# Optimization experiments

Hardware: AMD Instinct MI355X
Metric: run time of the kernel (lower is better)

Reference implementation:

```python
import jax, jax.numpy as jnp
import numpy as np

B, T, D, H, K, ED = 4, 1024, 512, 8, 30, 128
HD = D // H
SCALE = HD ** -0.5


def _ln(x, g, b, eps=1e-5):
    m = jnp.mean(x, axis=-1, keepdims=True)
    v = jnp.var(x, axis=-1, keepdims=True)
    return (x - m) / jnp.sqrt(v + eps) * g + b


def setup_inputs() -> dict:
    key = jax.random.key(0)
    ks = jax.random.split(key, 16)
    s = 0.02
    return {
        "h_V": jax.random.normal(ks[0], (B, T, D), jnp.float32),
        "k": jax.random.normal(ks[1], (B, T, D), jnp.float32),
        "v": jax.random.normal(ks[2], (B, T, D), jnp.float32),
        "E": jax.random.normal(ks[3], (B, T, K, ED), jnp.float32),
        "bias": jax.random.normal(ks[4], (B, T, T), jnp.float32),
        "Wq": jax.random.normal(ks[5], (D, D), jnp.float32) * s,
        "bq": jnp.zeros((D,), jnp.float32),
        "Wk": jax.random.normal(ks[6], (D, D), jnp.float32) * s,
        "bk": jnp.zeros((D,), jnp.float32),
        "Wv": jax.random.normal(ks[7], (D, D), jnp.float32) * s,
        "bv": jnp.zeros((D,), jnp.float32),
        "Wo": jax.random.normal(ks[8], (D, D + ED), jnp.float32) * s,
        "bo": jnp.zeros((D,), jnp.float32),
        "t": jax.random.normal(ks[9], (1,), jnp.float32),
        "gn": jnp.ones((D,), jnp.float32),
        "bn": jnp.zeros((D,), jnp.float32),
        "w1": jax.random.normal(ks[10], (4 * D, D), jnp.float32) * s,
        "bw1": jnp.zeros((4 * D,), jnp.float32),
        "w2": jax.random.normal(ks[11], (D, 4 * D), jnp.float32) * s,
        "bw2": jnp.zeros((D,), jnp.float32),
        "gf": jnp.ones((D,), jnp.float32),
        "bf": jnp.zeros((D,), jnp.float32),
        "g2": jnp.ones((D,), jnp.float32),
        "b2": jnp.zeros((D,), jnp.float32),
        "E_idx": jax.random.randint(ks[12], (B, T, K), 0, T),
        "mask": jax.random.randint(ks[13], (B, T), 0, 2).astype(jnp.int32),
    }


def reference(h_V, k, v, E, bias, Wq, bq, Wk, bk, Wv, bv, Wo, bo, t, gn, bn, w1, bw1, w2, bw2, gf, bf, g2, b2, E_idx, mask):
    # q/k/v projections; q scaled by head_dim**-0.5 (as in torch: q *= scaling)
    q = (h_V @ Wq.T + bq) * SCALE
    kk = k @ Wk.T + bk
    vv = v @ Wv.T + bv
    qh = q.reshape(B, T, H, HD)
    kh = kk.reshape(B, T, H, HD)
    vh = vv.reshape(B, T, H, HD)
    # attention logits with additive pairwise bias, broadcast over heads
    aw = jnp.einsum('bthd,bshd->bhts', qh, kh) + bias[:, None, :, :]
    aw = jnp.where(mask[:, None, None, :] == 0, -1e9, aw)
    # h_attend temperature scaling
    aw = aw / (4.0 ** jnp.tanh(t[0]))
    p = jax.nn.softmax(aw, axis=-1)  # [B,H,T,S]
    attn = jnp.einsum('bhts,bshd->bthd', p, vh).reshape(B, T, D)
    # edge path: head-mean attention, gather neighbor weights, weighted edge sum
    ma = jnp.mean(p, axis=1)                       # [B,T,S]
    g = jnp.take_along_axis(ma, E_idx, axis=-1)    # [B,T,K]
    edge = (g[..., None] * E).sum(axis=2) / (g.sum(axis=-1, keepdims=True) + 1e-6)  # [B,T,ED]
    out = jnp.concatenate([attn, edge], axis=-1) @ Wo.T + bo
    h = _ln(h_V + out, gn, bn, eps=1e-5)
    # PositionwiseFeedForward: residual + LN(eps=1e-6)
    ff = jax.nn.gelu(h @ w1.T + bw1, approximate=False) @ w2.T + bw2
    dh = _ln(h + ff, gf, bf, eps=1e-6)
    return _ln(h + dh, g2, b2, eps=1e-5)
```

## Files before the change

### kernel.cpp

```cpp
#include <hip/hip_runtime.h>
#include <hip/hip_fp16.h>
#include <math.h>

#define B_ 4
#define T_ 1024
#define D_ 512
#define H_ 8
#define HD_ 64
#define KN 30
#define ED_ 128
#define DFF_ 2048
#define M_ 4096
#define BH_ 32

typedef _Float16 f16;
typedef __attribute__((ext_vector_type(8))) _Float16 f16x8;
typedef __attribute__((ext_vector_type(4))) _Float16 f16x4;
typedef __attribute__((ext_vector_type(4))) float f32x4;

#define MFMA16 __builtin_amdgcn_mfma_f32_16x16x32_f16
#define LOG2E 1.44269504088896f

__device__ __forceinline__ f16x8 ld8(const f16* p){ return *reinterpret_cast<const f16x8*>(p); }

__device__ __forceinline__ void gld16(const void* g, void* l){
  __builtin_amdgcn_global_load_lds((const __attribute__((address_space(1))) void*)g,
                                   (__attribute__((address_space(3))) void*)l, 16, 0, 0);
}

struct CvtJobs {
  const float* s[9];
  f16* d[9];
  int start[10];
};

__global__ __launch_bounds__(256) void cvt9_kernel(CvtJobs J){
  const int blk = blockIdx.x;
  int j = 0;
  while (j < 8 && blk >= J.start[j+1]) ++j;
  const int i = (blk - J.start[j])*256 + threadIdx.x;
  float4 v = reinterpret_cast<const float4*>(J.s[j])[i];
  union { f16 h[4]; ushort4 u; } o;
  o.h[0]=(f16)v.x; o.h[1]=(f16)v.y; o.h[2]=(f16)v.z; o.h[3]=(f16)v.w;
  reinterpret_cast<ushort4*>(J.d[j])[i] = o.u;
}

__global__ __launch_bounds__(256) void biasprep_kernel(
    const float* __restrict__ bias, const int* __restrict__ mask,
    const float* __restrict__ tsc, f16* __restrict__ biasT)
{
  const int u = blockIdx.x*256 + threadIdx.x;
  const int l4 = u & 3, l16 = (u >> 2) & 15, qg = (u >> 6) & 1;
  const int ws = (u >> 7) & 3, c = (u >> 9) & 7, tb = (u >> 12) & 31, bi = u >> 17;
  const float s = exp2f(-2.0f*tanhf(tsc[0]))*LOG2E;
  const int t  = tb*32 + qg*16 + l16;
  const int s0 = c*128 + ws*32 + l4*4;
  const float* bp = bias + ((size_t)bi*T_ + t)*T_ + s0;
  const int*   mp = mask + bi*T_ + s0;
  union { f16 h[8]; f16x8 v8; } o;
#pragma unroll
  for (int st = 0; st < 2; ++st){
    float4 v = *reinterpret_cast<const float4*>(bp + st*16);
    int4  mm = *reinterpret_cast<const int4*>(mp + st*16);
    float x[4] = {v.x,v.y,v.z,v.w};
    int  m4[4] = {mm.x,mm.y,mm.z,mm.w};
#pragma unroll
    for (int j = 0; j < 4; ++j){
      float tv = (x[j] + (m4[j] ? 0.f : -60000.f))*s;
      o.h[st*4 + j] = (f16)fmaxf(tv, -60000.f);
    }
  }
  *reinterpret_cast<f16x8*>(biasT + (size_t)u*8) = o.v8;
}

template<int EPI>
__global__ __launch_bounds__(256,2) void gemm_tile(
    const f16* __restrict__ X, const f16* __restrict__ W,
    const float* __restrict__ bias, void* __restrict__ outp,
    int Kd, int ldo, int nbN)
{
  __shared__ f16 As[128*64];
  __shared__ f16 Bs[128*64];
  const int nwg = gridDim.x;
  const int bid = blockIdx.x;
  const int swz = (bid & 7)*(nwg >> 3) + (bid >> 3);
  const int mb = swz / nbN, nb = swz - mb*nbN;
  const int rb = mb*128, cb = nb*128;
  const int tid = threadIdx.x;
  const int w = tid >> 6, lane = tid & 63;
  const int l16 = lane & 15, l4 = lane >> 4;
  const int wr = w >> 1, wc = w & 1;
  const int key = l16 & 7;

  f32x4 acc[4][4];
#pragma unroll
  for (int m = 0; m < 4; ++m)
#pragma unroll
    for (int n = 0; n < 4; ++n) acc[m][n] = (f32x4){0.f,0.f,0.f,0.f};

  for (int k0 = 0; k0 < Kd; k0 += 64){
#pragma unroll
    for (int i = 0; i < 4; ++i){
      const int cidx = i*256 + w*64 + lane;
      const int r = cidx >> 3, p = cidx & 7;
      gld16(X + (size_t)(rb + r)*Kd + k0 + ((p ^ (r & 7)) << 3),
            &As[(i*256 + w*64)*8]);
      gld16(W + (size_t)(cb + r)*Kd + k0 + ((p ^ (r & 7)) << 3),
            &Bs[(i*256 + w*64)*8]);
    }
    __syncthreads();
#pragma unroll
    for (int kk = 0; kk < 2; ++kk){
      f16x8 a[4], b[4];
#pragma unroll
      for (int m = 0; m < 4; ++m)
        a[m] = ld8(&As[(wr*64 + m*16 + l16)*64 + (((kk*4 + l4) ^ key) << 3)]);
#pragma unroll
      for (int n = 0; n < 4; ++n)
        b[n] = ld8(&Bs[(wc*64 + n*16 + l16)*64 + (((kk*4 + l4) ^ key) << 3)]);
#pragma unroll
      for (int m = 0; m < 4; ++m)
#pragma unroll
        for (int n = 0; n < 4; ++n)
          acc[m][n] = MFMA16(a[m], b[n], acc[m][n], 0,0,0);
    }
    __syncthreads();
  }

#pragma unroll
  for (int n = 0; n < 4; ++n){
    const int col = cb + wc*64 + n*16 + l16;
    const float bv = bias[col];
#pragma unroll
    for (int m = 0; m < 4; ++m){
#pragma unroll
      for (int j = 0; j < 4; ++j){
        const int row = rb + wr*64 + m*16 + l4*4 + j;
        float v = acc[m][n][j] + bv;
        if (EPI == 1) v = 0.5f*v*(1.0f + erff(v*0.70710678118654752f));
        ((f16*)outp)[(size_t)row*ldo + col] = (f16)v;
      }
    }
  }
}

template<int EPI>
__global__ __launch_bounds__(256,2) void gemm_n64(
    const f16* __restrict__ X, const f16* __restrict__ W,
    const float* __restrict__ bias, void* __restrict__ outp,
    int Kd, int ldo, int nbN)
{
  __shared__ f16 As[128*64];
  __shared__ f16 Bs[64*64];
  const int nwg = gridDim.x;
  const int bid = blockIdx.x;
  const int swz = (bid & 7)*(nwg >> 3) + (bid >> 3);
  const int mb = swz / nbN, nb = swz - mb*nbN;
  const int rb = mb*128, cb = nb*64;
  const int tid = threadIdx.x;
  const int w = tid >> 6, lane = tid & 63;
  const int l16 = lane & 15, l4 = lane >> 4;
  const int wr = w >> 1, wc = w & 1;
  const int key = l16 & 7;

  f32x4 acc[4][2];
#pragma unroll
  for (int m = 0; m < 4; ++m)
#pragma unroll
    for (int n = 0; n < 2; ++n) acc[m][n] = (f32x4){0.f,0.f,0.f,0.f};

  for (int k0 = 0; k0 < Kd; k0 += 64){
#pragma unroll
    for (int i = 0; i < 4; ++i){
      const int cidx = i*256 + w*64 + lane;
      const int r = cidx >> 3, p = cidx & 7;
      gld16(X + (size_t)(rb + r)*Kd + k0 + ((p ^ (r & 7)) << 3),
            &As[(i*256 + w*64)*8]);
    }
#pragma unroll
    for (int i = 0; i < 2; ++i){
      const int cidx = i*256 + w*64 + lane;
      const int r = cidx >> 3, p = cidx & 7;
      gld16(W + (size_t)(cb + r)*Kd + k0 + ((p ^ (r & 7)) << 3),
            &Bs[(i*256 + w*64)*8]);
    }
    __syncthreads();
#pragma unroll
    for (int kk = 0; kk < 2; ++kk){
      f16x8 a[4], b[2];
#pragma unroll
      for (int m = 0; m < 4; ++m)
        a[m] = ld8(&As[(wr*64 + m*16 + l16)*64 + (((kk*4 + l4) ^ key) << 3)]);
#pragma unroll
      for (int n = 0; n < 2; ++n)
        b[n] = ld8(&Bs[(wc*32 + n*16 + l16)*64 + (((kk*4 + l4) ^ key) << 3)]);
#pragma unroll
      for (int m = 0; m < 4; ++m)
#pragma unroll
        for (int n = 0; n < 2; ++n)
          acc[m][n] = MFMA16(a[m], b[n], acc[m][n], 0,0,0);
    }
    __syncthreads();
  }

#pragma unroll
  for (int n = 0; n < 2; ++n){
    const int col = cb + wc*32 + n*16 + l16;
    const float bv = bias[col];
#pragma unroll
    for (int m = 0; m < 4; ++m){
#pragma unroll
      for (int j = 0; j < 4; ++j){
        const int row = rb + wr*64 + m*16 + l4*4 + j;
        float v = acc[m][n][j] + bv;
        if (EPI == 1) v = 0.5f*v*(1.0f + erff(v*0.70710678118654752f));
        ((f16*)outp)[(size_t)row*ldo + col] = (f16)v;
      }
    }
  }
}

__global__ __launch_bounds__(256,2) void qkv_tile(
    const f16* __restrict__ hV, const f16* __restrict__ kI, const f16* __restrict__ vI,
    const f16* __restrict__ Wq, const f16* __restrict__ Wk, const f16* __restrict__ Wv,
    const float* __restrict__ bq, const float* __restrict__ bk, const float* __restrict__ bv,
    const float* __restrict__ tsc,
    f16* __restrict__ qo, f16* __restrict__ ko, f16* __restrict__ vT)
{
  __shared__ f16 As[128*32];
  __shared__ f16 Bs[128*32];
  const int bid = blockIdx.x;
  const int swz = (bid & 7)*48 + (bid >> 3);
  const int g = swz >> 7;
  const int r = swz & 127;
  const int mb = r >> 2, nb = r & 3;
  const f16* X  = (g == 0) ? hV : ((g == 1) ? kI : vI);
  const f16* W  = (g == 0) ? Wq : ((g == 1) ? Wk : Wv);
  const float* bias = (g == 0) ? bq : ((g == 1) ? bk : bv);
  const int rb = mb*128, cb = nb*128;
  const int tid = threadIdx.x;
  const int w = tid >> 6, lane = tid & 63;
  const int l16 = lane & 15, l4 = lane >> 4;
  const int wr = w >> 1, wc = w & 1;
  const int sr = lane >> 2, sc = (lane & 3)*8;
  const f16* Ax0 = X + (size_t)(rb + w*16 + sr)*D_ + sc;
  const f16* Ax1 = X + (size_t)(rb + 64 + w*16 + sr)*D_ + sc;
  const f16* Bx0 = W + (size_t)(cb + w*16 + sr)*D_ + sc;
  const f16* Bx1 = W + (size_t)(cb + 64 + w*16 + sr)*D_ + sc;
  f16* Ad0 = &As[(w*16)*32];
  f16* Ad1 = &As[(64 + w*16)*32];
  f16* Bd0 = &Bs[(w*16)*32];
  f16* Bd1 = &Bs[(64 + w*16)*32];

  f32x4 acc[4][4];
#pragma unroll
  for (int m = 0; m < 4; ++m)
#pragma unroll
    for (int n = 0; n < 4; ++n) acc[m][n] = (f32x4){0.f,0.f,0.f,0.f};

  for (int k0 = 0; k0 < D_; k0 += 32){
    gld16(Ax0 + k0, Ad0);
    gld16(Ax1 + k0, Ad1);
    gld16(Bx0 + k0, Bd0);
    gld16(Bx1 + k0, Bd1);
    __syncthreads();
    f16x8 a[4], b[4];
#pragma unroll
    for (int m = 0; m < 4; ++m) a[m] = ld8(&As[(wr*64 + m*16 + l16)*32 + l4*8]);
#pragma unroll
    for (int n = 0; n < 4; ++n) b[n] = ld8(&Bs[(wc*64 + n*16 + l16)*32 + l4*8]);
#pragma unroll
    for (int m = 0; m < 4; ++m)
#pragma unroll
      for (int n = 0; n < 4; ++n)
        acc[m][n] = MFMA16(a[m], b[n], acc[m][n], 0,0,0);
    __syncthreads();
  }

  const float qs = exp2f(-2.0f*tanhf(tsc[0]))*LOG2E*0.125f;
  const float scale = (g == 0) ? qs : 1.0f;
  f16* out = (g == 0) ? qo : ko;
#pragma unroll
  for (int n = 0; n < 4; ++n){
    const int col = cb + wc*64 + n*16 + l16;
    const float bv = bias[col];
#pragma unroll
    for (int m = 0; m < 4; ++m){
#pragma unroll
      for (int j = 0; j < 4; ++j){
        const int row = rb + wr*64 + m*16 + l4*4 + j;
        const float v = (acc[m][n][j] + bv)*scale;
        if (g < 2){
          out[(size_t)row*D_ + col] = (f16)v;
        } else {
          const int b = row >> 10, t = row & (T_-1);
          const int h = col >> 6,  dl = col & (HD_-1);
          vT[(((size_t)b*H_ + h)*HD_ + dl)*T_ + t] = (f16)v;
        }
      }
    }
  }
}

__global__ __launch_bounds__(512,4) void attn_fused(
    const f16* __restrict__ q, const f16* __restrict__ k, const f16* __restrict__ vT,
    const f16* __restrict__ biasT, const int* __restrict__ eidx,
    f16* __restrict__ X2, float* __restrict__ gpart)
{
  __shared__ f16 Sb[16384];
  __shared__ f16 Pc[32*128];
  const int bid = blockIdx.x;
  const int swz = (bid & 7)*128 + (bid >> 3);
  const int bh = swz >> 5, tb = swz & 31;
  const int bi = bh >> 3, h = bh & 7;
  const int t0 = tb*32;
  const int tid = threadIdx.x, w = tid >> 6, lane = tid & 63;
  const int qg = w >> 2, ws = w & 3;
  const int l16 = lane & 15, l4 = lane >> 4;
  const int key = l16 & 7;

  const f16* qp = q + (size_t)(bi*T_ + t0 + qg*16 + l16)*D_ + h*HD_ + l4*8;
  const f16x8 q0 = ld8(qp), q1 = ld8(qp + 32);
  const f16* bb = biasT + (size_t)(bi*32 + tb)*32768 + ws*1024 + qg*512 + l16*32 + l4*8;
  f16x8 bfr[8];
#pragma unroll
  for (int c = 0; c < 8; ++c) bfr[c] = ld8(bb + c*4096);
  const int tl = tid & 255;
  int ga_r, ga_kk, ga_id, gb_r = 0, gb_kk = 0, gb_id = -1;
  ga_r = tl/KN; ga_kk = tl - ga_r*KN;
  ga_id = eidx[((size_t)(bi*T_ + t0 + qg*16 + ga_r))*KN + ga_kk];
  if (tl + 256 < 16*KN){
    gb_r = (tl+256)/KN; gb_kk = (tl+256) - gb_r*KN;
    gb_id = eidx[((size_t)(bi*T_ + t0 + qg*16 + gb_r))*KN + gb_kk];
  }

  const f16* kg = k + (size_t)(bi*T_)*D_ + h*HD_;
  const f16* vg = vT + (size_t)bh*HD_*T_;

  auto stageK = [&](int c, int slot){
#pragma unroll
    for (int i = 0; i < 2; ++i){
      const int cidx = i*512 + w*64 + lane;
      const int r = cidx >> 3, p = cidx & 7;
      gld16(kg + (size_t)(c*128 + r)*D_ + ((p ^ (r & 7)) << 3),
            &Sb[slot*8192 + (i*512 + w*64)*8]);
    }
  };
  auto stageV = [&](int sc, int slot){
#pragma unroll
    for (int i = 0; i < 2; ++i){
      const int cidx = i*512 + w*64 + lane;
      const int r = cidx >> 4, p = cidx & 15;
      gld16(vg + (size_t)r*T_ + sc*128 + ((p ^ (r & 7)) << 3),
            &Sb[slot*8192 + (i*512 + w*64)*8]);
    }
  };

  f32x4 acc[16];
  stageK(0, 0);
#pragma unroll
  for (int c = 0; c < 8; ++c){
    if (c < 7) stageK(c+1, (c+1)&1);
    if (c < 7) asm volatile("s_waitcnt vmcnt(2)" ::: "memory");
    else       asm volatile("s_waitcnt vmcnt(0)" ::: "memory");
    __builtin_amdgcn_sched_barrier(0);
    __builtin_amdgcn_s_barrier();
    __builtin_amdgcn_sched_barrier(0);
    const int base = (c&1)*8192;
#pragma unroll
    for (int step = 0; step < 2; ++step){
      const int rr = ws*32 + step*16 + l16;
      f32x4 a = {0.f,0.f,0.f,0.f};
      a = MFMA16(ld8(&Sb[base + rr*64 + ((l4 ^ key) << 3)]),       q0, a, 0,0,0);
      a = MFMA16(ld8(&Sb[base + rr*64 + (((4 + l4) ^ key) << 3)]), q1, a, 0,0,0);
#pragma unroll
      for (int j = 0; j < 4; ++j) a[j] += (float)bfr[c][step*4 + j];
      acc[c*2 + step] = a;
    }
    __builtin_amdgcn_s_barrier();
  }

  float* redf = (float*)Sb;
  float m = -3.4e38f;
#pragma unroll
  for (int c = 0; c < 16; ++c)
#pragma unroll
    for (int j = 0; j < 4; ++j) m = fmaxf(m, acc[c][j]);
  m = fmaxf(m, __shfl_xor(m, 16));
  m = fmaxf(m, __shfl_xor(m, 32));
  if (lane < 16) redf[(qg*4 + ws)*16 + lane] = m;
  __syncthreads();
  m = fmaxf(fmaxf(redf[(qg*4+0)*16 + l16], redf[(qg*4+1)*16 + l16]),
            fmaxf(redf[(qg*4+2)*16 + l16], redf[(qg*4+3)*16 + l16]));
  float l = 0.f;
#pragma unroll
  for (int c = 0; c < 16; ++c)
#pragma unroll
    for (int j = 0; j < 4; ++j){
      const float e = exp2f(acc[c][j] - m);
      l += e;
      acc[c][j] = e;
    }
  l += __shfl_xor(l, 16);
  l += __shfl_xor(l, 32);
  if (lane < 16) redf[128 + (qg*4 + ws)*16 + lane] = l;
  __syncthreads();
  const float lrq = redf[128 + (qg*4+0)*16 + l16] + redf[128 + (qg*4+1)*16 + l16]
                  + redf[128 + (qg*4+2)*16 + l16] + redf[128 + (qg*4+3)*16 + l16];
  __syncthreads();
  const float lr_a = __shfl(lrq, ga_r);
  const float lr_b = __shfl(lrq, gb_r);

  f32x4 oo0 = {0.f,0.f,0.f,0.f}, oo1 = oo0, oo2 = oo0, oo3 = oo0;
  float pva = 0.f, pvb = 0.f;
  stageV(0, 0);
#pragma unroll
  for (int sc = 0; sc < 8; ++sc){
#pragma unroll
    for (int step = 0; step < 2; ++step){
      const int slb = ws*32 + step*16 + l4*4;
      f16x4 pp;
#pragma unroll
      for (int j = 0; j < 4; ++j) pp[j] = (f16)acc[sc*2 + step][j];
      *reinterpret_cast<f16x4*>(
          &Pc[(qg*16 + l16)*128 + (((slb >> 3) ^ key) << 3) + (slb & 7)]) = pp;
    }
    if (sc < 7) stageV(sc+1, (sc+1)&1);
    if (sc < 7) asm volatile("s_waitcnt vmcnt(2) lgkmcnt(0)" ::: "memory");
    else        asm volatile("s_waitcnt vmcnt(0) lgkmcnt(0)" ::: "memory");
    __builtin_amdgcn_sched_barrier(0);
    __builtin_amdgcn_s_barrier();
    __builtin_amdgcn_sched_barrier(0);
    const int base = (sc&1)*8192;
    const int vrow = (ws*16 + l16)*128;
#pragma unroll
    for (int grp = 0; grp < 4; ++grp){
      const int ch = (grp*4 + l4) ^ key;
      const f16x8 pa = ld8(&Pc[(qg*16 + l16)*128 + (ch << 3)]);
      const f16x8 vb = ld8(&Sb[base + vrow + (ch << 3)]);
      if (grp == 0)      oo0 = MFMA16(pa, vb, oo0, 0,0,0);
      else if (grp == 1) oo1 = MFMA16(pa, vb, oo1, 0,0,0);
      else if (grp == 2) oo2 = MFMA16(pa, vb, oo2, 0,0,0);
      else               oo3 = MFMA16(pa, vb, oo3, 0,0,0);
    }
    if ((ga_id >> 7) == sc){
      const int r = qg*16 + ga_r;
      const int sl = ga_id & 127;
      pva = (float)Pc[r*128 + ((((sl >> 3) ^ (r & 7)) << 3) | (sl & 7))];
    }
    if (gb_id >= 0 && (gb_id >> 7) == sc){
      const int r = qg*16 + gb_r;
      const int sl = gb_id & 127;
      pvb = (float)Pc[r*128 + ((((sl >> 3) ^ (r & 7)) << 3) | (sl & 7))];
    }
    __builtin_amdgcn_s_barrier();
  }
  const f32x4 o = (oo0 + oo1) + (oo2 + oo3);

  gpart[((size_t)bh*T_ + t0 + qg*16 + ga_r)*KN + ga_kk] = pva/lr_a*0.125f;
  if (gb_id >= 0)
    gpart[((size_t)bh*T_ + t0 + qg*16 + gb_r)*KN + gb_kk] = pvb/lr_b*0.125f;

#pragma unroll
  for (int j = 0; j < 4; ++j){
    const float lr = __shfl(lrq, l4*4 + j);
    const int t = t0 + qg*16 + l4*4 + j;
    X2[((size_t)(bi*T_ + t))*640 + h*HD_ + ws*16 + l16] = (f16)(o[j]/lr);
  }
}

__global__ __launch_bounds__(128) void edge_kernel(
    const float* __restrict__ gpart, const float* __restrict__ E, f16* __restrict__ X2)
{
  __shared__ float gl[KN];
  __shared__ float ginv;
  const int bt = blockIdx.x;
  const int bi = bt >> 10, tt = bt & 1023;
  const int t = threadIdx.x;
  if (t < KN){
    float s = 0.f;
#pragma unroll
    for (int hh = 0; hh < H_; ++hh)
      s += gpart[((size_t)(bi*H_ + hh)*T_ + tt)*KN + t];
    gl[t] = s;
  }
  __syncthreads();
  if (t == 0){
    float s = 0.f;
#pragma unroll
    for (int i = 0; i < KN; ++i) s += gl[i];
    ginv = 1.0f/(s + 1e-6f);
  }
  __syncthreads();
  float acc = 0.f;
  const float* Ep = E + (size_t)bt*KN*ED_ + t;
#pragma unroll 5
  for (int kk = 0; kk < KN; ++kk) acc += gl[kk]*Ep[(size_t)kk*ED_];
  X2[(size_t)bt*640 + 512 + t] = (f16)(acc*ginv);
}

__device__ __forceinline__ float block_sum(float v, float* sbuf){
  for (int o = 32; o; o >>= 1) v += __shfl_down(v, o);
  __syncthreads();
  if ((threadIdx.x & 63) == 0) sbuf[threadIdx.x >> 6] = v;
  __syncthreads();
  return sbuf[0]+sbuf[1]+sbuf[2]+sbuf[3];
}

__global__ __launch_bounds__(256) void ln1_kernel(
    const float* __restrict__ hV, const f16* __restrict__ hraw,
    const float* __restrict__ gn, const float* __restrict__ bn,
    f16* __restrict__ hh)
{
  __shared__ float sbuf[4];
  const int r = blockIdx.x, t = threadIdx.x;
  const size_t base = (size_t)r*D_;
  float x0 = hV[base+t]     + (float)hraw[base+t];
  float x1 = hV[base+t+256] + (float)hraw[base+t+256];
  float s = block_sum(x0+x1, sbuf);
  const float mean = s*(1.f/512.f);
  float d0 = x0-mean, d1 = x1-mean;
  float vs = block_sum(d0*d0+d1*d1, sbuf);
  const float rstd = rsqrtf(vs*(1.f/512.f) + 1e-5f);
  hh[base+t]     = (f16)(d0*rstd*gn[t]     + bn[t]);
  hh[base+t+256] = (f16)(d1*rstd*gn[t+256] + bn[t+256]);
}

__global__ __launch_bounds__(256) void final_kernel(
    const f16* __restrict__ hh, const f16* __restrict__ ffr,
    const float* __restrict__ gf, const float* __restrict__ bfv,
    const float* __restrict__ g2, const float* __restrict__ b2,
    float* __restrict__ out)
{
  __shared__ float sbuf[4];
  const int r = blockIdx.x, t = threadIdx.x;
  const size_t base = (size_t)r*D_;
  const float h0 = (float)hh[base+t], h1 = (float)hh[base+t+256];
  float x0 = h0 + (float)ffr[base+t], x1 = h1 + (float)ffr[base+t+256];
  float s = block_sum(x0+x1, sbuf);
  float mean = s*(1.f/512.f);
  float d0 = x0-mean, d1 = x1-mean;
  float vs = block_sum(d0*d0+d1*d1, sbuf);
  float rstd = rsqrtf(vs*(1.f/512.f) + 1e-6f);
  const float dh0 = d0*rstd*gf[t]     + bfv[t];
  const float dh1 = d1*rstd*gf[t+256] + bfv[t+256];
  const float y0 = h0 + dh0, y1 = h1 + dh1;
  s = block_sum(y0+y1, sbuf);
  mean = s*(1.f/512.f);
  d0 = y0-mean; d1 = y1-mean;
  vs = block_sum(d0*d0+d1*d1, sbuf);
  rstd = rsqrtf(vs*(1.f/512.f) + 1e-5f);
  out[base+t]     = d0*rstd*g2[t]     + b2[t];
  out[base+t+256] = d1*rstd*g2[t+256] + b2[t+256];
}

extern "C" void kernel_launch(void* const* d_in, const int* in_sizes, int n_in,
                              void* d_out, int out_size, void* d_ws, size_t ws_size,
                              hipStream_t stream)
{
  (void)in_sizes; (void)n_in; (void)out_size;
  const float* h_V  = (const float*)d_in[0];
  const float* kin  = (const float*)d_in[1];
  const float* vin  = (const float*)d_in[2];
  const float* E    = (const float*)d_in[3];
  const float* bias = (const float*)d_in[4];
  const float* Wq   = (const float*)d_in[5];
  const float* bq   = (const float*)d_in[6];
  const float* Wk   = (const float*)d_in[7];
  const float* bk   = (const float*)d_in[8];
  const float* Wv   = (const float*)d_in[9];
  const float* bv   = (const float*)d_in[10];
  const float* Wo   = (const float*)d_in[11];
  const float* bo   = (const float*)d_in[12];
  const float* tsc  = (const float*)d_in[13];
  const float* gn   = (const float*)d_in[14];
  const float* bn   = (const float*)d_in[15];
  const float* w1   = (const float*)d_in[16];
  const float* bw1  = (const float*)d_in[17];
  const float* w2   = (const float*)d_in[18];
  const float* bw2  = (const float*)d_in[19];
  const float* gf   = (const float*)d_in[20];
  const float* bfv  = (const float*)d_in[21];
  const float* g2   = (const float*)d_in[22];
  const float* b2   = (const float*)d_in[23];
  const int*   Eidx = (const int*)d_in[24];
  const int*   mask = (const int*)d_in[25];
  float* out = (float*)d_out;

  char* wsb = (char*)d_ws;
  size_t off = 0;
  auto alloc = [&](size_t bytes) -> void* {
    void* pp = wsb + off; off += (bytes + 255) & ~(size_t)255; return pp;
  };
  f16* hVb  = (f16*)alloc((size_t)M_*D_*2);
  f16* kbI  = (f16*)alloc((size_t)M_*D_*2);
  f16* vbI  = (f16*)alloc((size_t)M_*D_*2);
  f16* Wqb  = (f16*)alloc((size_t)D_*D_*2);
  f16* Wkb  = (f16*)alloc((size_t)D_*D_*2);
  f16* Wvb  = (f16*)alloc((size_t)D_*D_*2);
  f16* Wob  = (f16*)alloc((size_t)D_*(D_+ED_)*2);
  f16* w1b  = (f16*)alloc((size_t)DFF_*D_*2);
  f16* w2b  = (f16*)alloc((size_t)D_*DFF_*2);
  f16* qb   = (f16*)alloc((size_t)M_*D_*2);
  f16* kb   = (f16*)alloc((size_t)M_*D_*2);
  f16* vT   = (f16*)alloc((size_t)M_*D_*2);
  f16* biasT= (f16*)alloc((size_t)B_*T_*T_*2);
  f16* X2   = (f16*)alloc((size_t)M_*640*2);
  float* gpart = (float*)alloc((size_t)BH_*T_*KN*4);
  f16* hraw = (f16*)alloc((size_t)M_*D_*2);
  f16* hh   = (f16*)alloc((size_t)M_*D_*2);
  f16* ff1  = (f16*)alloc((size_t)M_*DFF_*2);
  if (ws_size < off) return;
  f16* ffraw = hraw;

  {
    CvtJobs J;
    const float* srcs[9] = {h_V, kin, vin, Wq, Wk, Wv, Wo, w1, w2};
    f16* dsts[9] = {hVb, kbI, vbI, Wqb, Wkb, Wvb, Wob, w1b, w2b};
    const int n4s[9] = {M_*D_/4, M_*D_/4, M_*D_/4, D_*D_/4, D_*D_/4, D_*D_/4,
                        D_*(D_+ED_)/4, DFF_*D_/4, D_*DFF_/4};
    int cum = 0;
    for (int i = 0; i < 9; ++i){
      J.s[i] = srcs[i]; J.d[i] = dsts[i]; J.start[i] = cum;
      cum += n4s[i]/256;
    }
    J.start[9] = cum;
    cvt9_kernel<<<cum,256,0,stream>>>(J);
  }
  biasprep_kernel<<<2048,256,0,stream>>>(bias, mask, tsc, biasT);

  qkv_tile<<<384,256,0,stream>>>(hVb, kbI, vbI, Wqb, Wkb, Wvb, bq, bk, bv, tsc, qb, kb, vT);

  attn_fused<<<1024,512,0,stream>>>(qb, kb, vT, biasT, Eidx, X2, gpart);

  edge_kernel<<<M_,128,0,stream>>>(gpart, E, X2);

  gemm_n64<2><<<256,256,0,stream>>>(X2, Wob, bo, hraw, D_+ED_, D_, 8);
  ln1_kernel<<<M_,256,0,stream>>>(h_V, hraw, gn, bn, hh);

  gemm_tile<1><<<512,256,0,stream>>>(hh, w1b, bw1, ff1, D_, DFF_, 16);
  gemm_n64<2><<<256,256,0,stream>>>(ff1, w2b, bw2, ffraw, DFF_, D_, 8);

  final_kernel<<<M_,256,0,stream>>>(hh, ffraw, gf, bfv, g2, b2, out);
}
```

Baseline: 162.3 us.

## Merge conversion and bias-prep launches; widen QKV K-tile with XOR-swizzled LDS

The fp32-to-fp16 conversion kernel and the bias/mask preparation kernel are folded into one launch, with the first blocks doing conversion and the rest doing bias prep, which removes one kernel launch and its tail. The QKV projection GEMM now stages a 64-wide K slice per iteration instead of 32. This halves the number of barrier pairs, and the XOR swizzle on the LDS column chunk is meant to avoid bank conflicts on the 128-byte rows. The cost is doubled LDS per block, which may affect occupancy under launch_bounds(256,2).

```diff
diff --git a/kernel.cpp b/kernel.cpp
--- a/kernel.cpp
+++ b/kernel.cpp
@@ -34,22 +34,23 @@
   int start[10];
 };
 
-__global__ __launch_bounds__(256) void cvt9_kernel(CvtJobs J){
-  const int blk = blockIdx.x;
-  int j = 0;
-  while (j < 8 && blk >= J.start[j+1]) ++j;
-  const int i = (blk - J.start[j])*256 + threadIdx.x;
-  float4 v = reinterpret_cast<const float4*>(J.s[j])[i];
-  union { f16 h[4]; ushort4 u; } o;
-  o.h[0]=(f16)v.x; o.h[1]=(f16)v.y; o.h[2]=(f16)v.z; o.h[3]=(f16)v.w;
-  reinterpret_cast<ushort4*>(J.d[j])[i] = o.u;
-}
-
-__global__ __launch_bounds__(256) void biasprep_kernel(
+__global__ __launch_bounds__(256) void prep_kernel(
+    CvtJobs J, int cvtBlocks,
     const float* __restrict__ bias, const int* __restrict__ mask,
     const float* __restrict__ tsc, f16* __restrict__ biasT)
 {
-  const int u = blockIdx.x*256 + threadIdx.x;
+  if (blockIdx.x < cvtBlocks){
+    const int blk = blockIdx.x;
+    int j = 0;
+    while (j < 8 && blk >= J.start[j+1]) ++j;
+    const int i = (blk - J.start[j])*256 + threadIdx.x;
+    float4 v = reinterpret_cast<const float4*>(J.s[j])[i];
+    union { f16 h[4]; ushort4 u; } o;
+    o.h[0]=(f16)v.x; o.h[1]=(f16)v.y; o.h[2]=(f16)v.z; o.h[3]=(f16)v.w;
+    reinterpret_cast<ushort4*>(J.d[j])[i] = o.u;
+    return;
+  }
+  const int u = (blockIdx.x - cvtBlocks)*256 + threadIdx.x;
   const int l4 = u & 3, l16 = (u >> 2) & 15, qg = (u >> 6) & 1;
   const int ws = (u >> 7) & 3, c = (u >> 9) & 7, tb = (u >> 12) & 31, bi = u >> 17;
   const float s = exp2f(-2.0f*tanhf(tsc[0]))*LOG2E;
@@ -227,8 +228,8 @@
     const float* __restrict__ tsc,
     f16* __restrict__ qo, f16* __restrict__ ko, f16* __restrict__ vT)
 {
-  __shared__ f16 As[128*32];
-  __shared__ f16 Bs[128*32];
+  __shared__ f16 As[128*64];
+  __shared__ f16 Bs[128*64];
   const int bid = blockIdx.x;
   const int swz = (bid & 7)*48 + (bid >> 3);
   const int g = swz >> 7;
@@ -242,15 +243,7 @@
   const int w = tid >> 6, lane = tid & 63;
   const int l16 = lane & 15, l4 = lane >> 4;
   const int wr = w >> 1, wc = w & 1;
-  const int sr = lane >> 2, sc = (lane & 3)*8;
-  const f16* Ax0 = X + (size_t)(rb + w*16 + sr)*D_ + sc;
-  const f16* Ax1 = X + (size_t)(rb + 64 + w*16 + sr)*D_ + sc;
-  const f16* Bx0 = W + (size_t)(cb + w*16 + sr)*D_ + sc;
-  const f16* Bx1 = W + (size_t)(cb + 64 + w*16 + sr)*D_ + sc;
-  f16* Ad0 = &As[(w*16)*32];
-  f16* Ad1 = &As[(64 + w*16)*32];
-  f16* Bd0 = &Bs[(w*16)*32];
-  f16* Bd1 = &Bs[(64 + w*16)*32];
+  const int key = l16 & 7;
 
   f32x4 acc[4][4];
 #pragma unroll
@@ -258,22 +251,32 @@
 #pragma unroll
     for (int n = 0; n < 4; ++n) acc[m][n] = (f32x4){0.f,0.f,0.f,0.f};
 
-  for (int k0 = 0; k0 < D_; k0 += 32){
-    gld16(Ax0 + k0, Ad0);
-    gld16(Ax1 + k0, Ad1);
-    gld16(Bx0 + k0, Bd0);
-    gld16(Bx1 + k0, Bd1);
+  for (int k0 = 0; k0 < D_; k0 += 64){
+#pragma unroll
+    for (int i = 0; i < 4; ++i){
+      const int cidx = i*256 + w*64 + lane;
+      const int rr = cidx >> 3, p = cidx & 7;
+      gld16(X + (size_t)(rb + rr)*D_ + k0 + ((p ^ (rr & 7)) << 3),
+            &As[(i*256 + w*64)*8]);
+      gld16(W + (size_t)(cb + rr)*D_ + k0 + ((p ^ (rr & 7)) << 3),
+            &Bs[(i*256 + w*64)*8]);
+    }
     __syncthreads();
-    f16x8 a[4], b[4];
-#pragma unroll
-    for (int m = 0; m < 4; ++m) a[m] = ld8(&As[(wr*64 + m*16 + l16)*32 + l4*8]);
-#pragma unroll
-    for (int n = 0; n < 4; ++n) b[n] = ld8(&Bs[(wc*64 + n*16 + l16)*32 + l4*8]);
-#pragma unroll
-    for (int m = 0; m < 4; ++m)
+#pragma unroll
+    for (int kk = 0; kk < 2; ++kk){
+      f16x8 a[4], b[4];
+#pragma unroll
+      for (int m = 0; m < 4; ++m)
+        a[m] = ld8(&As[(wr*64 + m*16 + l16)*64 + (((kk*4 + l4) ^ key) << 3)]);
 #pragma unroll
       for (int n = 0; n < 4; ++n)
-        acc[m][n] = MFMA16(a[m], b[n], acc[m][n], 0,0,0);
+        b[n] = ld8(&Bs[(wc*64 + n*16 + l16)*64 + (((kk*4 + l4) ^ key) << 3)]);
+#pragma unroll
+      for (int m = 0; m < 4; ++m)
+#pragma unroll
+        for (int n = 0; n < 4; ++n)
+          acc[m][n] = MFMA16(a[m], b[n], acc[m][n], 0,0,0);
+    }
     __syncthreads();
   }
 
@@ -625,9 +628,8 @@
       cum += n4s[i]/256;
     }
     J.start[9] = cum;
-    cvt9_kernel<<<cum,256,0,stream>>>(J);
-  }
-  biasprep_kernel<<<2048,256,0,stream>>>(bias, mask, tsc, biasT);
+    prep_kernel<<<cum + 2048,256,0,stream>>>(J, cum, bias, mask, tsc, biasT);
+  }
 
   qkv_tile<<<384,256,0,stream>>>(hVb, kbI, vbI, Wqb, Wkb, Wvb, bq, bk, bv, tsc, qb, kb, vT);
 
```

Result: no change. 159.3 us (-1.9%).
